# Optimization experiments

Hardware: AMD Instinct MI355X
Metric: run time of the kernel (lower is better)

## Reference

```python
import jax, jax.numpy as jnp
import numpy as np

N_NODES = 100000
N_EDGES = 625000
D = 128
DEPTH = 2
BN_EPS = 1e-5


def setup_inputs() -> dict:
    key = jax.random.key(0)
    ks = jax.random.split(key, 8)
    x = jax.random.normal(ks[0], (N_NODES, D), dtype=jnp.float32)
    edge_index = jax.random.randint(ks[1], (2, N_EDGES), 0, N_NODES, dtype=jnp.int64)
    edge_weight = jax.random.uniform(ks[2], (N_EDGES,), dtype=jnp.float32)
    s = 1.0 / np.sqrt(D)
    W_lin = jax.random.uniform(ks[3], (DEPTH, D, D), jnp.float32, -s, s)
    W_gcn = jax.random.uniform(ks[4], (DEPTH, D, D), jnp.float32, -s, s)
    gamma = jnp.ones((DEPTH, D), jnp.float32)
    beta = jnp.zeros((DEPTH, D), jnp.float32)
    return {"x": x, "edge_index": edge_index, "edge_weight": edge_weight,
            "W_lin": W_lin, "W_gcn": W_gcn, "gamma": gamma, "beta": beta}


def reference(x, edge_index, edge_weight, W_lin, W_gcn, gamma, beta):
    n = x.shape[0]
    row, col = edge_index[0], edge_index[1]  # source, target
    # gcn_norm with add_self_loops=False: deg over targets, symmetric normalization
    deg = jax.ops.segment_sum(edge_weight, col, num_segments=n)
    dinv = jnp.where(deg > 0, jax.lax.rsqrt(deg), 0.0)
    norm = dinv[row] * edge_weight * dinv[col]  # [E]

    for i in range(DEPTH):
        hl = x @ W_lin[i].T                       # parallel linear branch
        hg = x @ W_gcn[i].T                       # GCNConv linear
        msg = norm[:, None] * hg[row]             # [E, D] messages
        hr = jax.ops.segment_sum(msg, col, num_segments=n)
        h = hl + hr
        # BatchNorm1d, training mode (batch statistics, biased variance)
        mu = jnp.mean(h, axis=0)
        var = jnp.mean((h - mu) ** 2, axis=0)
        h = (h - mu) * jax.lax.rsqrt(var + BN_EPS) * gamma[i] + beta[i]
        x = jnp.maximum(h, 0.0) if i != DEPTH - 1 else h
    return x
```

## Files before the change

kernel.cpp:

```cpp
#include <hip/hip_runtime.h>

#define NN 100000
#define NE 625000
#define DD 128
#define CAP 32
#define NREP 8

#define CONVB 12500
#define WPACKB 256
#define FILL4B ((NE / 4 + 255) / 256)
#define GB ((NN + 63) / 64)

typedef __attribute__((ext_vector_type(8))) short bf16x8;
typedef __attribute__((ext_vector_type(4))) float f32x4;

static __device__ __forceinline__ unsigned short f2bf(float f) {
    union { float f; unsigned u; } v; v.f = f;
    unsigned u = v.u + 0x7fffu + ((v.u >> 16) & 1u);
    return (unsigned short)(u >> 16);
}
static __device__ __forceinline__ float bflo(unsigned u) { return __uint_as_float(u << 16); }
static __device__ __forceinline__ float bfhi(unsigned u) { return __uint_as_float(u & 0xffff0000u); }

static __device__ __forceinline__ void foldLDS(const float* __restrict__ stats,
                                               const float* __restrict__ gamma,
                                               const float* __restrict__ beta,
                                               float* sSc, float* sSh, int t) {
    if (t < 128) {
        float sum = 0.f, sq = 0.f;
        #pragma unroll
        for (int rp = 0; rp < NREP; rp++) {
            sum += stats[rp * 256 + t];
            sq  += stats[rp * 256 + 128 + t];
        }
        float mu = sum * (1.0f / NN);
        float var = sq * (1.0f / NN) - mu * mu;
        float is = rsqrtf(var + 1e-5f);
        float sc = is * gamma[t];
        sSc[t] = sc;
        sSh[t] = beta[t] - mu * sc;
    }
}

__global__ __launch_bounds__(256) void k_pre(const float* __restrict__ x,
                                             unsigned* __restrict__ Xb2,
                                             const float* __restrict__ Wl,
                                             const float* __restrict__ Wg,
                                             unsigned short* __restrict__ wp,
                                             const int* __restrict__ row,
                                             const int* __restrict__ col,
                                             const float* __restrict__ w,
                                             int* __restrict__ cd,
                                             int2* __restrict__ ebuf) {
    int b = blockIdx.x, t = threadIdx.x;
    if (b < FILL4B) {
        int id = b * 256 + t;
        if (id < NE / 4) {
            int e = id * 4;
            int4 rr = *(const int4*)&row[e];
            int4 cc = *(const int4*)&col[e];
            float4 ww = *(const float4*)&w[e];
            int p0 = atomicAdd(&cd[2 * cc.x], 1);
            int p1 = atomicAdd(&cd[2 * cc.y], 1);
            int p2 = atomicAdd(&cd[2 * cc.z], 1);
            int p3 = atomicAdd(&cd[2 * cc.w], 1);
            atomicAdd((float*)&cd[2 * cc.x + 1], ww.x);
            atomicAdd((float*)&cd[2 * cc.y + 1], ww.y);
            atomicAdd((float*)&cd[2 * cc.z + 1], ww.z);
            atomicAdd((float*)&cd[2 * cc.w + 1], ww.w);
            if (p0 < CAP) { int2 v; v.x = rr.x; v.y = __float_as_int(ww.x); ebuf[(size_t)cc.x * CAP + p0] = v; }
            if (p1 < CAP) { int2 v; v.x = rr.y; v.y = __float_as_int(ww.y); ebuf[(size_t)cc.y * CAP + p1] = v; }
            if (p2 < CAP) { int2 v; v.x = rr.z; v.y = __float_as_int(ww.z); ebuf[(size_t)cc.z * CAP + p2] = v; }
            if (p3 < CAP) { int2 v; v.x = rr.w; v.y = __float_as_int(ww.w); ebuf[(size_t)cc.w * CAP + p3] = v; }
        }
    } else if (b < FILL4B + WPACKB) {
        int idx = (b - FILL4B) * 256 + t;
        int l = idx >> 15;
        int rem = idx & 32767;
        int n = rem >> 8;
        int k = rem & 255;
        float v = (k < 128) ? Wl[(size_t)l * DD * DD + n * DD + k]
                            : Wg[(size_t)l * DD * DD + n * DD + (k - 128)];
        int wv = n >> 5;
        int tt = (n >> 4) & 1;
        int i  = n & 15;
        int ss = k >> 5;
        int q  = (k >> 3) & 3;
        int j  = k & 7;
        size_t off = ((size_t)((((l * 4 + wv) * 2 + tt) * 8 + ss)) * 64 + q * 16 + i) * 8 + j;
        wp[off] = f2bf(v);
    } else {
        size_t i = (size_t)(b - FILL4B - WPACKB) * 256 + t;
        size_t base = i * 4;
        float4 v = *(const float4*)&x[base];
        uint2 o;
        o.x = (unsigned)f2bf(v.x) | ((unsigned)f2bf(v.y) << 16);
        o.y = (unsigned)f2bf(v.z) | ((unsigned)f2bf(v.w) << 16);
        *(uint2*)&Xb2[i * 2] = o;
    }
}

__global__ __launch_bounds__(256) void k_dinv(const int* __restrict__ cd,
                                              float* __restrict__ dinv) {
    int i = blockIdx.x * 256 + threadIdx.x;
    if (i < NN) {
        float dg = __int_as_float(cd[2 * i + 1]);
        dinv[i] = (dg > 0.f) ? rsqrtf(dg) : 0.f;
    }
}

template<int LAYER>
__global__ __launch_bounds__(256) void k_gatherP(const int* __restrict__ cd,
                                                 const int2* __restrict__ ebuf,
                                                 const float* __restrict__ dinv,
                                                 const unsigned* __restrict__ X2,
                                                 const float* __restrict__ stats,
                                                 const float* __restrict__ gamma,
                                                 const float* __restrict__ beta,
                                                 unsigned* __restrict__ P2) {
    __shared__ float sSc[128], sSh[128];
    int t = threadIdx.x;
    int node = blockIdx.x * 4 + (t >> 6);
    int lane = t & 63;
    float scx = 0.f, scy = 0.f, shx = 0.f, shy = 0.f;
    if (LAYER) {
        foldLDS(stats, gamma, beta, sSc, sSh, t);
        __syncthreads();
        scx = sSc[2 * lane]; scy = sSc[2 * lane + 1];
        shx = sSh[2 * lane]; shy = sSh[2 * lane + 1];
    }
    int c = cd[2 * node]; if (c > CAP) c = CAP;
    const int2* eb = ebuf + (size_t)node * CAP;
    float dn = dinv[node];
    float ax = 0.f, ay = 0.f;
    int p = 0;
    for (; p + 3 < c; p += 4) {
        int2 e0 = eb[p], e1 = eb[p + 1], e2 = eb[p + 2], e3 = eb[p + 3];
        float w0 = __int_as_float(e0.y) * dinv[e0.x];
        float w1 = __int_as_float(e1.y) * dinv[e1.x];
        float w2 = __int_as_float(e2.y) * dinv[e2.x];
        float w3 = __int_as_float(e3.y) * dinv[e3.x];
        unsigned u0 = X2[(size_t)e0.x * 64 + lane];
        unsigned u1 = X2[(size_t)e1.x * 64 + lane];
        unsigned u2 = X2[(size_t)e2.x * 64 + lane];
        unsigned u3 = X2[(size_t)e3.x * 64 + lane];
        float x0 = bflo(u0), y0 = bfhi(u0);
        float x1 = bflo(u1), y1 = bfhi(u1);
        float x2 = bflo(u2), y2 = bfhi(u2);
        float x3 = bflo(u3), y3 = bfhi(u3);
        if (LAYER) {
            x0 = fmaxf(x0 * scx + shx, 0.f); y0 = fmaxf(y0 * scy + shy, 0.f);
            x1 = fmaxf(x1 * scx + shx, 0.f); y1 = fmaxf(y1 * scy + shy, 0.f);
            x2 = fmaxf(x2 * scx + shx, 0.f); y2 = fmaxf(y2 * scy + shy, 0.f);
            x3 = fmaxf(x3 * scx + shx, 0.f); y3 = fmaxf(y3 * scy + shy, 0.f);
        }
        ax += w0 * x0 + w1 * x1 + w2 * x2 + w3 * x3;
        ay += w0 * y0 + w1 * y1 + w2 * y2 + w3 * y3;
    }
    for (; p < c; p++) {
        int2 e0 = eb[p];
        float w0 = __int_as_float(e0.y) * dinv[e0.x];
        unsigned u0 = X2[(size_t)e0.x * 64 + lane];
        float x0 = bflo(u0), y0 = bfhi(u0);
        if (LAYER) {
            x0 = fmaxf(x0 * scx + shx, 0.f); y0 = fmaxf(y0 * scy + shy, 0.f);
        }
        ax += w0 * x0;
        ay += w0 * y0;
    }
    ax *= dn; ay *= dn;
    P2[(size_t)node * 64 + lane] = (unsigned)f2bf(ax) | ((unsigned)f2bf(ay) << 16);
}

template<int LAYER>
__global__ __launch_bounds__(256) void k_gemm_s(const unsigned short* Xin,
                                                const unsigned short* P,
                                                const unsigned short* __restrict__ wp,
                                                const float* __restrict__ statsIn,
                                                const float* __restrict__ gammaIn,
                                                const float* __restrict__ betaIn,
                                                unsigned short* Hout,
                                                float* __restrict__ statsOut) {
    __shared__ __align__(16) char smem[34816];
    unsigned short* sAv = (unsigned short*)smem;
    unsigned short* sBv = (unsigned short*)smem;
    float* red = (float*)(smem + 17408);
    float* sSc = (float*)(smem + 33792);
    float* sSh = (float*)(smem + 34304);

    const int t = threadIdx.x;
    const int wave = t >> 6;
    const int lane = t & 63;
    const int i16 = lane & 15;
    const int quad = lane >> 4;
    const int rowBase = blockIdx.x * 64;

    if (LAYER == 1) {
        foldLDS(statsIn, gammaIn, betaIn, sSc, sSh, t);
        __syncthreads();
    }

    bf16x8 wf[2][8];
    #pragma unroll
    for (int tt = 0; tt < 2; tt++)
        #pragma unroll
        for (int ss = 0; ss < 8; ss++) {
            size_t off = ((size_t)(((wave * 2 + tt) * 8 + ss)) * 64 + quad * 16 + i16) * 8;
            wf[tt][ss] = *(const bf16x8*)&wp[off];
        }

    #pragma unroll
    for (int rep = 0; rep < 4; rep++) {
        int lin = rep * 2048 + t * 8;
        int r = lin >> 7, c = lin & 127;
        int rr = rowBase + r; if (rr >= NN) rr = NN - 1;
        uint4 u = *(const uint4*)&Xin[(size_t)rr * DD + c];
        if (LAYER == 1) {
            float4 sc0 = *(const float4*)&sSc[c];
            float4 sc1 = *(const float4*)&sSc[c + 4];
            float4 sh0 = *(const float4*)&sSh[c];
            float4 sh1 = *(const float4*)&sSh[c + 4];
            float v0 = fmaxf(bflo(u.x) * sc0.x + sh0.x, 0.f);
            float v1 = fmaxf(bfhi(u.x) * sc0.y + sh0.y, 0.f);
            float v2 = fmaxf(bflo(u.y) * sc0.z + sh0.z, 0.f);
            float v3 = fmaxf(bfhi(u.y) * sc0.w + sh0.w, 0.f);
            float v4 = fmaxf(bflo(u.z) * sc1.x + sh1.x, 0.f);
            float v5 = fmaxf(bfhi(u.z) * sc1.y + sh1.y, 0.f);
            float v6 = fmaxf(bflo(u.w) * sc1.z + sh1.z, 0.f);
            float v7 = fmaxf(bfhi(u.w) * sc1.w + sh1.w, 0.f);
            u.x = (unsigned)f2bf(v0) | ((unsigned)f2bf(v1) << 16);
            u.y = (unsigned)f2bf(v2) | ((unsigned)f2bf(v3) << 16);
            u.z = (unsigned)f2bf(v4) | ((unsigned)f2bf(v5) << 16);
            u.w = (unsigned)f2bf(v6) | ((unsigned)f2bf(v7) << 16);
        }
        *(uint4*)&sAv[r * 264 + c] = u;
    }
    #pragma unroll
    for (int rep = 0; rep < 4; rep++) {
        int lin = rep * 2048 + t * 8;
        int r = lin >> 7, c = lin & 127;
        int rr = rowBase + r; if (rr >= NN) rr = NN - 1;
        uint4 u = *(const uint4*)&P[(size_t)rr * DD + c];
        *(uint4*)&sAv[r * 264 + 128 + c] = u;
    }
    __syncthreads();

    f32x4 acc[4][2] = {{{0.f,0.f,0.f,0.f}}};
    #pragma unroll
    for (int ss = 0; ss < 8; ss++) {
        bf16x8 af[4];
        #pragma unroll
        for (int mt = 0; mt < 4; mt++)
            af[mt] = *(const bf16x8*)&sAv[(mt * 16 + i16) * 264 + ss * 32 + quad * 8];
        #pragma unroll
        for (int mt = 0; mt < 4; mt++)
            #pragma unroll
            for (int tt = 0; tt < 2; tt++)
                acc[mt][tt] = __builtin_amdgcn_mfma_f32_16x16x32_bf16(
                    af[mt], wf[tt][ss], acc[mt][tt], 0, 0, 0);
    }

    __syncthreads();
    #pragma unroll
    for (int mt = 0; mt < 4; mt++)
        #pragma unroll
        for (int r = 0; r < 4; r++) {
            int row = mt * 16 + quad * 4 + r;
            #pragma unroll
            for (int tt = 0; tt < 2; tt++)
                sBv[row * 136 + wave * 32 + tt * 16 + i16] = f2bf(acc[mt][tt][r]);
        }
    __syncthreads();

    float s[8] = {0.f,0.f,0.f,0.f,0.f,0.f,0.f,0.f};
    float q[8] = {0.f,0.f,0.f,0.f,0.f,0.f,0.f,0.f};
    const int cg = t & 15;
    #pragma unroll
    for (int it = 0; it < 4; it++) {
        int row = it * 16 + (t >> 4);
        int gr = rowBase + row;
        uint4 v = *(const uint4*)&sBv[row * 136 + cg * 8];
        float m = (gr < NN) ? 1.f : 0.f;
        if (gr < NN) *(uint4*)&Hout[(size_t)gr * DD + cg * 8] = v;
        float e0 = bflo(v.x) * m, e1 = bfhi(v.x) * m;
        float e2 = bflo(v.y) * m, e3 = bfhi(v.y) * m;
        float e4 = bflo(v.z) * m, e5 = bfhi(v.z) * m;
        float e6 = bflo(v.w) * m, e7 = bfhi(v.w) * m;
        s[0] += e0; q[0] += e0 * e0;  s[1] += e1; q[1] += e1 * e1;
        s[2] += e2; q[2] += e2 * e2;  s[3] += e3; q[3] += e3 * e3;
        s[4] += e4; q[4] += e4 * e4;  s[5] += e5; q[5] += e5 * e5;
        s[6] += e6; q[6] += e6 * e6;  s[7] += e7; q[7] += e7 * e7;
    }
    {
        int ro = t >> 4;
        #pragma unroll
        for (int j = 0; j < 8; j++) {
            red[(ro * 16 + cg) * 16 + j]     = s[j];
            red[(ro * 16 + cg) * 16 + 8 + j] = q[j];
        }
    }
    __syncthreads();
    {
        int colx = t & 127;
        int type = t >> 7;
        float tot = 0.f;
        #pragma unroll
        for (int ro = 0; ro < 16; ro++)
            tot += red[(ro * 16 + (colx >> 3)) * 16 + type * 8 + (colx & 7)];
        atomicAdd(&statsOut[(blockIdx.x & (NREP - 1)) * 256 + type * 128 + colx], tot);
    }
}

__global__ __launch_bounds__(256) void k_apply_out(const unsigned* __restrict__ H2,
                                                   const float* __restrict__ stats,
                                                   const float* __restrict__ gamma,
                                                   const float* __restrict__ beta,
                                                   float* __restrict__ out) {
    __shared__ __align__(16) float sSc[128];
    __shared__ __align__(16) float sSh[128];
    int t = threadIdx.x;
    foldLDS(stats, gamma, beta, sSc, sSh, t);
    __syncthreads();
    size_t i = (size_t)blockIdx.x * 256 + t;
    size_t base = i * 4;
    int c = (int)(base & 127);
    uint2 u = *(const uint2*)&H2[i * 2];
    float4 sc = *(const float4*)&sSc[c];
    float4 sh = *(const float4*)&sSh[c];
    float4 o;
    o.x = bflo(u.x) * sc.x + sh.x;
    o.y = bfhi(u.x) * sc.y + sh.y;
    o.z = bflo(u.y) * sc.z + sh.z;
    o.w = bfhi(u.y) * sc.w + sh.w;
    *(float4*)&out[base] = o;
}

extern "C" void kernel_launch(void* const* d_in, const int* in_sizes, int n_in,
                              void* d_out, int out_size, void* d_ws, size_t ws_size,
                              hipStream_t stream) {
    const float* x_in  = (const float*)d_in[0];
    const int*   ei    = (const int*)d_in[1];
    const float* ew    = (const float*)d_in[2];
    const float* Wl    = (const float*)d_in[3];
    const float* Wg    = (const float*)d_in[4];
    const float* gamma = (const float*)d_in[5];
    const float* beta  = (const float*)d_in[6];
    float* out = (float*)d_out;

    char* p = (char*)d_ws;
    unsigned short* bufA = (unsigned short*)p; p += (size_t)NN * DD * 2;
    unsigned short* bufB = (unsigned short*)p; p += (size_t)NN * DD * 2;
    int2* ebuf  = (int2*)p;  p += (size_t)NN * CAP * 8;
    int*   cd     = (int*)p;   p += (size_t)NN * 8;
    float* stats0 = (float*)p; p += NREP * 256 * 4;
    float* stats1 = (float*)p; p += NREP * 256 * 4;
    float* dinv   = (float*)p; p += 400000;
    unsigned short* wpack = (unsigned short*)p; p += 65536 * 2;

    const int* row = ei;
    const int* col = ei + NE;

    hipMemsetAsync(cd, 0, (size_t)NN * 8 + 2 * NREP * 256 * 4, stream);
    k_pre<<<FILL4B + WPACKB + CONVB, 256, 0, stream>>>(
        x_in, (unsigned*)bufA, Wl, Wg, wpack, row, col, ew, cd, ebuf);
    k_dinv<<<(NN + 255) / 256, 256, 0, stream>>>(cd, dinv);

    k_gatherP<0><<<NN / 4, 256, 0, stream>>>(cd, ebuf, dinv, (const unsigned*)bufA,
                                             nullptr, nullptr, nullptr, (unsigned*)bufB);
    k_gemm_s<0><<<GB, 256, 0, stream>>>(bufA, bufB, wpack,
                                        nullptr, nullptr, nullptr, bufA, stats0);

    k_gatherP<1><<<NN / 4, 256, 0, stream>>>(cd, ebuf, dinv, (const unsigned*)bufA,
                                             stats0, gamma, beta, (unsigned*)bufB);
    k_gemm_s<1><<<GB, 256, 0, stream>>>(bufA, bufB, wpack + 32768,
                                        stats0, gamma, beta, bufB, stats1);

    k_apply_out<<<NN * DD / 1024, 256, 0, stream>>>((const unsigned*)bufB, stats1,
                                                    gamma + DD, beta + DD, out);
}
```

Measured before the change: 325.2 us.

## Drop float degree atomics, compute dinv from CSR buckets, two nodes per wave

The fill kernel now does only the integer count atomic per edge and processes two edges per thread. The float atomic for weighted degree is gone, and degree is recomputed from the bucketed edge weights by 8 lanes per node in a new dinv kernel. The gather kernel now has each wave handle two nodes with interleaved 4-edge chunks, which raises memory-level parallelism. One side effect is that degree now ignores edges beyond CAP, the same as the gather does, which may differ from the reference when a node has more than 32 in-edges.

```diff
diff --git a/kernel.cpp b/kernel.cpp
--- a/kernel.cpp
+++ b/kernel.cpp
@@ -8,7 +8,7 @@
 
 #define CONVB 12500
 #define WPACKB 256
-#define FILL4B ((NE / 4 + 255) / 256)
+#define FILL2B ((NE / 2 + 255) / 256)
 #define GB ((NN + 63) / 64)
 
 typedef __attribute__((ext_vector_type(8))) short bf16x8;
@@ -50,31 +50,29 @@
                                              const int* __restrict__ row,
                                              const int* __restrict__ col,
                                              const float* __restrict__ w,
-                                             int* __restrict__ cd,
+                                             int* __restrict__ cnt,
                                              int2* __restrict__ ebuf) {
     int b = blockIdx.x, t = threadIdx.x;
-    if (b < FILL4B) {
+    if (b < FILL2B) {
         int id = b * 256 + t;
-        if (id < NE / 4) {
-            int e = id * 4;
-            int4 rr = *(const int4*)&row[e];
-            int4 cc = *(const int4*)&col[e];
-            float4 ww = *(const float4*)&w[e];
-            int p0 = atomicAdd(&cd[2 * cc.x], 1);
-            int p1 = atomicAdd(&cd[2 * cc.y], 1);
-            int p2 = atomicAdd(&cd[2 * cc.z], 1);
-            int p3 = atomicAdd(&cd[2 * cc.w], 1);
-            atomicAdd((float*)&cd[2 * cc.x + 1], ww.x);
-            atomicAdd((float*)&cd[2 * cc.y + 1], ww.y);
-            atomicAdd((float*)&cd[2 * cc.z + 1], ww.z);
-            atomicAdd((float*)&cd[2 * cc.w + 1], ww.w);
-            if (p0 < CAP) { int2 v; v.x = rr.x; v.y = __float_as_int(ww.x); ebuf[(size_t)cc.x * CAP + p0] = v; }
-            if (p1 < CAP) { int2 v; v.x = rr.y; v.y = __float_as_int(ww.y); ebuf[(size_t)cc.y * CAP + p1] = v; }
-            if (p2 < CAP) { int2 v; v.x = rr.z; v.y = __float_as_int(ww.z); ebuf[(size_t)cc.z * CAP + p2] = v; }
-            if (p3 < CAP) { int2 v; v.x = rr.w; v.y = __float_as_int(ww.w); ebuf[(size_t)cc.w * CAP + p3] = v; }
-        }
-    } else if (b < FILL4B + WPACKB) {
-        int idx = (b - FILL4B) * 256 + t;
+        if (id < NE / 2) {
+            int e = id * 2;
+            int2 rr = *(const int2*)&row[e];
+            int2 cc = *(const int2*)&col[e];
+            float2 ww = *(const float2*)&w[e];
+            int p0 = atomicAdd(&cnt[cc.x], 1);
+            int p1 = atomicAdd(&cnt[cc.y], 1);
+            if (p0 < CAP) {
+                int2 v; v.x = rr.x; v.y = __float_as_int(ww.x);
+                ebuf[(size_t)cc.x * CAP + p0] = v;
+            }
+            if (p1 < CAP) {
+                int2 v; v.x = rr.y; v.y = __float_as_int(ww.y);
+                ebuf[(size_t)cc.y * CAP + p1] = v;
+            }
+        }
+    } else if (b < FILL2B + WPACKB) {
+        int idx = (b - FILL2B) * 256 + t;
         int l = idx >> 15;
         int rem = idx & 32767;
         int n = rem >> 8;
@@ -90,7 +88,7 @@
         size_t off = ((size_t)((((l * 4 + wv) * 2 + tt) * 8 + ss)) * 64 + q * 16 + i) * 8 + j;
         wp[off] = f2bf(v);
     } else {
-        size_t i = (size_t)(b - FILL4B - WPACKB) * 256 + t;
+        size_t i = (size_t)(b - FILL2B - WPACKB) * 256 + t;
         size_t base = i * 4;
         float4 v = *(const float4*)&x[base];
         uint2 o;
@@ -100,17 +98,23 @@
     }
 }
 
-__global__ __launch_bounds__(256) void k_dinv(const int* __restrict__ cd,
-                                              float* __restrict__ dinv) {
-    int i = blockIdx.x * 256 + threadIdx.x;
-    if (i < NN) {
-        float dg = __int_as_float(cd[2 * i + 1]);
-        dinv[i] = (dg > 0.f) ? rsqrtf(dg) : 0.f;
-    }
+__global__ __launch_bounds__(256) void k_dinvb(const int* __restrict__ cnt,
+                                               const int2* __restrict__ ebuf,
+                                               float* __restrict__ dinv) {
+    int t = threadIdx.x;
+    int node = blockIdx.x * 32 + (t >> 3);
+    int l = t & 7;
+    int c = cnt[node]; if (c > CAP) c = CAP;
+    float s = 0.f;
+    for (int p = l; p < c; p += 8) s += __int_as_float(ebuf[(size_t)node * CAP + p].y);
+    s += __shfl_down(s, 4, 8);
+    s += __shfl_down(s, 2, 8);
+    s += __shfl_down(s, 1, 8);
+    if (l == 0) dinv[node] = (s > 0.f) ? rsqrtf(s) : 0.f;
 }
 
 template<int LAYER>
-__global__ __launch_bounds__(256) void k_gatherP(const int* __restrict__ cd,
+__global__ __launch_bounds__(256) void k_gatherP(const int* __restrict__ cnt,
                                                  const int2* __restrict__ ebuf,
                                                  const float* __restrict__ dinv,
                                                  const unsigned* __restrict__ X2,
@@ -119,9 +123,9 @@
                                                  const float* __restrict__ beta,
                                                  unsigned* __restrict__ P2) {
     __shared__ float sSc[128], sSh[128];
-    int t = threadIdx.x;
-    int node = blockIdx.x * 4 + (t >> 6);
-    int lane = t & 63;
+    const int t = threadIdx.x;
+    const int wave = t >> 6;
+    const int lane = t & 63;
     float scx = 0.f, scy = 0.f, shx = 0.f, shy = 0.f;
     if (LAYER) {
         foldLDS(stats, gamma, beta, sSc, sSh, t);
@@ -129,12 +133,16 @@
         scx = sSc[2 * lane]; scy = sSc[2 * lane + 1];
         shx = sSh[2 * lane]; shy = sSh[2 * lane + 1];
     }
-    int c = cd[2 * node]; if (c > CAP) c = CAP;
-    const int2* eb = ebuf + (size_t)node * CAP;
-    float dn = dinv[node];
-    float ax = 0.f, ay = 0.f;
-    int p = 0;
-    for (; p + 3 < c; p += 4) {
+
+    const int node0 = blockIdx.x * 8 + wave * 2;
+    const int node1 = node0 + 1;
+    int c0 = cnt[node0]; if (c0 > CAP) c0 = CAP;
+    int c1 = cnt[node1]; if (c1 > CAP) c1 = CAP;
+    const int2* eb0 = ebuf + (size_t)node0 * CAP;
+    const int2* eb1 = ebuf + (size_t)node1 * CAP;
+    float ax0 = 0.f, ay0 = 0.f, ax1 = 0.f, ay1 = 0.f;
+
+    auto chunk4 = [&](const int2* __restrict__ eb, int p, float& ax, float& ay) {
         int2 e0 = eb[p], e1 = eb[p + 1], e2 = eb[p + 2], e3 = eb[p + 3];
         float w0 = __int_as_float(e0.y) * dinv[e0.x];
         float w1 = __int_as_float(e1.y) * dinv[e1.x];
@@ -156,8 +164,8 @@
         }
         ax += w0 * x0 + w1 * x1 + w2 * x2 + w3 * x3;
         ay += w0 * y0 + w1 * y1 + w2 * y2 + w3 * y3;
-    }
-    for (; p < c; p++) {
+    };
+    auto edge1 = [&](const int2* __restrict__ eb, int p, float& ax, float& ay) {
         int2 e0 = eb[p];
         float w0 = __int_as_float(e0.y) * dinv[e0.x];
         unsigned u0 = X2[(size_t)e0.x * 64 + lane];
@@ -167,9 +175,25 @@
         }
         ax += w0 * x0;
         ay += w0 * y0;
-    }
-    ax *= dn; ay *= dn;
-    P2[(size_t)node * 64 + lane] = (unsigned)f2bf(ax) | ((unsigned)f2bf(ay) << 16);
+    };
+
+    const int mc = (c0 < c1) ? c0 : c1;
+    int p = 0;
+    for (; p + 3 < mc; p += 4) {
+        chunk4(eb0, p, ax0, ay0);
+        chunk4(eb1, p, ax1, ay1);
+    }
+    int p0 = p, p1 = p;
+    for (; p0 + 3 < c0; p0 += 4) chunk4(eb0, p0, ax0, ay0);
+    for (; p0 < c0; p0++)        edge1(eb0, p0, ax0, ay0);
+    for (; p1 + 3 < c1; p1 += 4) chunk4(eb1, p1, ax1, ay1);
+    for (; p1 < c1; p1++)        edge1(eb1, p1, ax1, ay1);
+
+    float dn0 = dinv[node0], dn1 = dinv[node1];
+    ax0 *= dn0; ay0 *= dn0;
+    ax1 *= dn1; ay1 *= dn1;
+    P2[(size_t)node0 * 64 + lane] = (unsigned)f2bf(ax0) | ((unsigned)f2bf(ay0) << 16);
+    P2[(size_t)node1 * 64 + lane] = (unsigned)f2bf(ax1) | ((unsigned)f2bf(ay1) << 16);
 }
 
 template<int LAYER>
@@ -351,7 +375,7 @@
     unsigned short* bufA = (unsigned short*)p; p += (size_t)NN * DD * 2;
     unsigned short* bufB = (unsigned short*)p; p += (size_t)NN * DD * 2;
     int2* ebuf  = (int2*)p;  p += (size_t)NN * CAP * 8;
-    int*   cd     = (int*)p;   p += (size_t)NN * 8;
+    int*   cnt    = (int*)p;   p += (size_t)NN * 4;
     float* stats0 = (float*)p; p += NREP * 256 * 4;
     float* stats1 = (float*)p; p += NREP * 256 * 4;
     float* dinv   = (float*)p; p += 400000;
@@ -360,17 +384,17 @@
     const int* row = ei;
     const int* col = ei + NE;
 
-    hipMemsetAsync(cd, 0, (size_t)NN * 8 + 2 * NREP * 256 * 4, stream);
-    k_pre<<<FILL4B + WPACKB + CONVB, 256, 0, stream>>>(
-        x_in, (unsigned*)bufA, Wl, Wg, wpack, row, col, ew, cd, ebuf);
-    k_dinv<<<(NN + 255) / 256, 256, 0, stream>>>(cd, dinv);
-
-    k_gatherP<0><<<NN / 4, 256, 0, stream>>>(cd, ebuf, dinv, (const unsigned*)bufA,
+    hipMemsetAsync(cnt, 0, (size_t)NN * 4 + 2 * NREP * 256 * 4, stream);
+    k_pre<<<FILL2B + WPACKB + CONVB, 256, 0, stream>>>(
+        x_in, (unsigned*)bufA, Wl, Wg, wpack, row, col, ew, cnt, ebuf);
+    k_dinvb<<<NN / 32, 256, 0, stream>>>(cnt, ebuf, dinv);
+
+    k_gatherP<0><<<NN / 8, 256, 0, stream>>>(cnt, ebuf, dinv, (const unsigned*)bufA,
                                              nullptr, nullptr, nullptr, (unsigned*)bufB);
     k_gemm_s<0><<<GB, 256, 0, stream>>>(bufA, bufB, wpack,
                                         nullptr, nullptr, nullptr, bufA, stats0);
 
-    k_gatherP<1><<<NN / 4, 256, 0, stream>>>(cd, ebuf, dinv, (const unsigned*)bufA,
+    k_gatherP<1><<<NN / 8, 256, 0, stream>>>(cnt, ebuf, dinv, (const unsigned*)bufA,
                                              stats0, gamma, beta, (unsigned*)bufB);
     k_gemm_s<1><<<GB, 256, 0, stream>>>(bufA, bufB, wpack + 32768,
                                         stats0, gamma, beta, bufB, stats1);
```

New measurement: 292.2 us. 10.1% less time.
